# Kernel tuning notes

Hardware: AMD Instinct MI355X
Metric: run time of the kernel (lower is better)

Reference implementation:

```python
import jax, jax.numpy as jnp
import numpy as np

B, N, D = 2, 2048, 1024
H = 16
HD = D // H  # 64
NEG = -1e30


def setup_inputs() -> dict:
    key = jax.random.key(0)
    ks = jax.random.split(key, 6)
    s = 0.02
    return {
        "x": jax.random.normal(ks[0], (B, N, D), dtype=jnp.float32),
        "Wq": jax.random.normal(ks[1], (D, D), dtype=jnp.float32) * s,
        "Wk": jax.random.normal(ks[2], (D, D), dtype=jnp.float32) * s,
        "Wv": jax.random.normal(ks[3], (D, D), dtype=jnp.float32) * s,
        "Wo": jax.random.normal(ks[4], (D, D), dtype=jnp.float32) * s,
        "Wf": jax.random.normal(ks[5], (D, H), dtype=jnp.float32) * s,
    }


def reference(x, Wq, Wk, Wv, Wo, Wf):
    b, n, d = x.shape
    h, hd = H, HD
    scale = hd ** -0.5
    # projections (Linear without bias; weights stored as [in, out])
    q = (x @ Wq).reshape(b, n, h, hd).transpose(0, 2, 1, 3)  # b h n hd
    k = (x @ Wk).reshape(b, n, h, hd).transpose(0, 2, 1, 3)
    v = (x @ Wv).reshape(b, n, h, hd).transpose(0, 2, 1, 3)
    # per-head log forget gate, cumulative sum over positions
    log_f = jax.nn.log_sigmoid(x @ Wf).transpose(0, 2, 1)  # b h n
    c = jnp.cumsum(log_f, axis=-1)  # b h n
    # scores with additive decay bias: bias[i,j] = c[i] - c[j] (j <= i)
    scores = jnp.einsum('bhid,bhjd->bhij', q, k) * scale
    scores = scores + c[..., :, None] - c[..., None, :]
    causal = jnp.tril(jnp.ones((n, n), dtype=bool))
    scores = jnp.where(causal, scores, NEG)
    attn = jax.nn.softmax(scores, axis=-1)
    out = jnp.einsum('bhij,bhjd->bhid', attn, v)  # b h n hd
    out = out.transpose(0, 2, 1, 3).reshape(b, n, d)
    return out @ Wo
```

## Files before the change

### kernel.cpp

```cpp
#include <hip/hip_runtime.h>
#include <hip/hip_bf16.h>
#include <stdint.h>

#define NN 2048
#define DD 1024
#define HH 16
#define HDD 64
#define QBLK 64
#define KVBLK 64

typedef unsigned short u16;
typedef __attribute__((ext_vector_type(8))) __bf16 bf16x8_t;
typedef __attribute__((ext_vector_type(4))) float f32x4_t;

static __device__ __forceinline__ u16 f2bf(float f) {
  union { float f; uint32_t u; } v; v.f = f;
  uint32_t r = v.u + 0x7FFFu + ((v.u >> 16) & 1u);
  return (u16)(r >> 16);
}

static __device__ __forceinline__ uint32_t packbf2(float a, float b) {
  __hip_bfloat162 h2 = __float22bfloat162_rn(make_float2(a, b));
  union { __hip_bfloat162 hh; uint32_t u; } cvt; cvt.hh = h2;
  return cvt.u;
}

static __device__ __forceinline__ void async_copy16(const void* g, void* l) {
  __builtin_amdgcn_global_load_lds((const __attribute__((address_space(1))) void*)g,
                                   (__attribute__((address_space(3))) void*)l, 16, 0, 0);
}

__global__ void transpose_w_kernel(const float* __restrict__ W0, const float* __restrict__ W1,
                                   const float* __restrict__ W2, const float* __restrict__ W3,
                                   u16* __restrict__ Wt) {
  __shared__ float tile[64][65];
  const float* W = blockIdx.y == 0 ? W0 : blockIdx.y == 1 ? W1 : blockIdx.y == 2 ? W2 : W3;
  u16* out = Wt + (size_t)blockIdx.y * DD * DD;
  int bx = blockIdx.x & 15;
  int by = blockIdx.x >> 4;
  int t = threadIdx.x;
  int c = t & 63, r4 = t >> 6;
#pragma unroll
  for (int i = 0; i < 16; i++) {
    int row = i * 4 + r4;
    tile[row][c] = W[(by * 64 + row) * DD + bx * 64 + c];
  }
  __syncthreads();
#pragma unroll
  for (int i = 0; i < 16; i++) {
    int row = i * 4 + r4;
    out[(bx * 64 + row) * DD + by * 64 + c] = f2bf(tile[c][row]);
  }
}

__global__ void logf_kernel(const float* __restrict__ x, const float* __restrict__ Wf,
                            float* __restrict__ lf, u16* __restrict__ xb) {
  __shared__ float xs[DD];
  __shared__ float part[16][17];
  int row = blockIdx.x;
  int t = threadIdx.x;
  float4 v = *(const float4*)&x[(size_t)row * DD + t * 4];
  *(float4*)&xs[t * 4] = v;
  ushort4 o;
  o.x = f2bf(v.x); o.y = f2bf(v.y); o.z = f2bf(v.z); o.w = f2bf(v.w);
  *(ushort4*)&xb[(size_t)row * DD + t * 4] = o;
  __syncthreads();
  int h = t & 15, chunk = t >> 4;
  float s = 0.f;
#pragma unroll 8
  for (int e = 0; e < 64; e++)
    s += xs[chunk * 64 + e] * Wf[(chunk * 64 + e) * HH + h];
  part[chunk][h] = s;
  __syncthreads();
  if (t < 16) {
    float z = 0.f;
#pragma unroll
    for (int i = 0; i < 16; i++) z += part[i][t];
    float ls = fminf(z, 0.f) - log1pf(__expf(-fabsf(z)));
    int b = row >> 11, n = row & (NN - 1);
    lf[(b * HH + t) * NN + n] = ls;
  }
}

__global__ void cumsum_kernel(const float* __restrict__ lf, float* __restrict__ c) {
  int bh = blockIdx.x;
  int lane = threadIdx.x;
  const float* in = lf + bh * NN;
  float* out = c + bh * NN;
  float carry = 0.f;
  for (int t0 = 0; t0 < NN; t0 += 256) {
    float4 v = *(const float4*)&in[t0 + lane * 4];
    float s1 = v.x + v.y, s2 = s1 + v.z, s3 = s2 + v.w;
    float incl = s3;
#pragma unroll
    for (int off = 1; off < 64; off <<= 1) {
      float u = __shfl_up(incl, off, 64);
      if (lane >= off) incl += u;
    }
    float excl = incl - s3 + carry;
    float4 o;
    o.x = excl + v.x; o.y = excl + s1; o.z = excl + s2; o.w = excl + s3;
    *(float4*)&out[t0 + lane * 4] = o;
    carry = __shfl(incl, 63, 64) + carry;
  }
}

__global__ __launch_bounds__(512, 4) void gemm_kernel(const u16* __restrict__ A,
                                                      const u16* __restrict__ Wt,
                                                      u16* __restrict__ oQ, u16* __restrict__ oK,
                                                      u16* __restrict__ oV, float* __restrict__ oF,
                                                      int mode) {
  __shared__ u16 Als[128 * 64];
  __shared__ u16 Bls[128 * 64];
  int m0 = blockIdx.y * 128, n0 = blockIdx.x * 128;
  int tid = threadIdx.x;
  int lane = tid & 63, w = tid >> 6;
  int wm = w >> 2, wn = w & 3;
  int lr = lane & 15, lg = lane >> 4;

  const u16* gA[2]; const u16* gB[2]; u16* lA[2]; u16* lB[2];
#pragma unroll
  for (int j = 0; j < 2; j++) {
    int s = tid + j * 512;
    int row = s >> 3, ch = s & 7;
    int scol = (ch ^ (row & 7)) * 8;
    gA[j] = &A [(size_t)(m0 + row) * DD + scol];
    gB[j] = &Wt[(size_t)(n0 + row) * DD + scol];
    lA[j] = &Als[s * 8];
    lB[j] = &Bls[s * 8];
  }

  f32x4_t acc[4][2];
#pragma unroll
  for (int i = 0; i < 4; i++)
#pragma unroll
    for (int j = 0; j < 2; j++) acc[i][j] = (f32x4_t){0.f, 0.f, 0.f, 0.f};

  for (int kt = 0; kt < DD; kt += 64) {
    __syncthreads();
#pragma unroll
    for (int j = 0; j < 2; j++) {
      async_copy16(gA[j] + kt, lA[j]);
      async_copy16(gB[j] + kt, lB[j]);
    }
    __syncthreads();
#pragma unroll
    for (int kk = 0; kk < 2; kk++) {
      bf16x8_t af[4], bfv[2];
#pragma unroll
      for (int mi = 0; mi < 4; mi++) {
        int row = wm * 64 + mi * 16 + lr;
        int boff = (row * 128 + kk * 64 + lg * 16) ^ ((row & 7) << 4);
        af[mi] = *(const bf16x8_t*)((const char*)Als + boff);
      }
#pragma unroll
      for (int ni = 0; ni < 2; ni++) {
        int row = wn * 32 + ni * 16 + lr;
        int boff = (row * 128 + kk * 64 + lg * 16) ^ ((row & 7) << 4);
        bfv[ni] = *(const bf16x8_t*)((const char*)Bls + boff);
      }
#pragma unroll
      for (int mi = 0; mi < 4; mi++)
#pragma unroll
        for (int ni = 0; ni < 2; ni++)
          acc[mi][ni] = __builtin_amdgcn_mfma_f32_16x16x32_bf16(af[mi], bfv[ni], acc[mi][ni], 0, 0, 0);
    }
  }

  if (mode == 1) {
#pragma unroll
    for (int mi = 0; mi < 4; mi++)
#pragma unroll
      for (int ni = 0; ni < 2; ni++) {
        int gcol = n0 + wn * 32 + ni * 16 + lr;
#pragma unroll
        for (int r = 0; r < 4; r++) {
          int grow = m0 + wm * 64 + mi * 16 + lg * 4 + r;
          oF[(size_t)grow * DD + gcol] = acc[mi][ni][r];
        }
      }
  } else {
    int which = n0 >> 10;
    u16* outp = which == 0 ? oQ : which == 1 ? oK : oV;
    int nl0 = n0 & 1023;
#pragma unroll
    for (int mi = 0; mi < 4; mi++)
#pragma unroll
      for (int ni = 0; ni < 2; ni++) {
        int gcol = nl0 + wn * 32 + ni * 16 + lr;
        int h = gcol >> 6, hd = gcol & 63;
#pragma unroll
        for (int r = 0; r < 4; r++) {
          int grow = m0 + wm * 64 + mi * 16 + lg * 4 + r;
          int b = grow >> 11, n = grow & (NN - 1);
          outp[((size_t)(b * HH + h) * NN + n) * HDD + hd] = f2bf(acc[mi][ni][r]);
        }
      }
  }
}

__global__ void transpose_v_kernel(const u16* __restrict__ Vtmp, u16* __restrict__ Vt) {
  __shared__ u16 tile[64][80];
  int bh = blockIdx.y;
  int n0 = blockIdx.x * 64;
  int t = threadIdx.x;
  const u16* src = Vtmp + (size_t)bh * NN * HDD;
  u16* dst = Vt + (size_t)bh * HDD * NN;
#pragma unroll
  for (int it = 0; it < 2; it++) {
    int cc = t + it * 256;
    int row = cc >> 3, p = cc & 7;
    *(uint4*)&tile[row][p * 8] = *(const uint4*)&src[(size_t)(n0 + row) * HDD + p * 8];
  }
  __syncthreads();
#pragma unroll
  for (int it = 0; it < 2; it++) {
    int cc = t + it * 256;
    int row = cc >> 3, p = cc & 7;
    union { u16 v[8]; uint4 q; } tmp;
#pragma unroll
    for (int e = 0; e < 8; e++) tmp.v[e] = tile[p * 8 + e][row];
    *(uint4*)&dst[(size_t)row * NN + n0 + p * 8] = tmp.q;
  }
}

__global__ __launch_bounds__(256) void attn_kernel(const u16* __restrict__ Q,
                                                   const u16* __restrict__ K,
                                                   const u16* __restrict__ Vt,
                                                   const float* __restrict__ cw,
                                                   u16* __restrict__ O) {
  __shared__ u16 Kls[2][KVBLK * 64];
  __shared__ u16 Vls[2][64 * KVBLK];
  int flat = blockIdx.y * gridDim.x + blockIdx.x;
  int swz = (flat & 7) * 64 + (flat >> 3);
  int pidx = swz & 15, bh = swz >> 4;
  int tid = threadIdx.x;
  int lane = tid & 63, w = tid >> 6;
  int lr = lane & 15, lg = lane >> 4;
  const u16* Qh = Q + (size_t)bh * NN * HDD;
  const u16* Kh = K + (size_t)bh * NN * HDD;
  const u16* Vh = Vt + (size_t)bh * HDD * NN;
  const float* ch = cw + bh * NN;
  int b = bh >> 4, h = bh & 15;

  int s0 = tid, s1 = tid + 256;
  int r0 = s0 >> 3, p0 = s0 & 7;
  int r1 = s1 >> 3, p1 = s1 & 7;
  const u16* gk0 = &Kh[(size_t)r0 * HDD + ((p0 ^ (r0 & 7)) * 8)];
  const u16* gk1 = &Kh[(size_t)r1 * HDD + ((p1 ^ (r1 & 7)) * 8)];
  const u16* gv0 = &Vh[(size_t)r0 * NN + ((p0 ^ (r0 & 7)) * 8)];
  const u16* gv1 = &Vh[(size_t)r1 * NN + ((p1 ^ (r1 & 7)) * 8)];

  for (int which = 0; which < 2; which++) {
    int tile = which == 0 ? (31 - pidx) : pidx;
    int qb = tile * QBLK + w * 16;
    int iq = qb + lr;

    bf16x8_t qf[2];
#pragma unroll
    for (int s = 0; s < 2; s++)
      qf[s] = *(const bf16x8_t*)&Qh[(size_t)iq * HDD + s * 32 + lg * 8];
    float cq = ch[iq];

    float lsum = 0.f;
    f32x4_t oacc[4];
#pragma unroll
    for (int fn = 0; fn < 4; fn++) oacc[fn] = (f32x4_t){0.f, 0.f, 0.f, 0.f};

    async_copy16(gk0, &Kls[0][s0 * 8]);
    async_copy16(gk1, &Kls[0][s1 * 8]);
    async_copy16(gv0, &Vls[0][s0 * 8]);
    async_copy16(gv1, &Vls[0][s1 * 8]);
    __syncthreads();

    int cur = 0;
    for (int kvt = 0; kvt <= tile; kvt++) {
      if (kvt < tile) {
        int nb = cur ^ 1;
        size_t kvn = (size_t)(kvt + 1) * KVBLK;
        async_copy16(gk0 + kvn * HDD, &Kls[nb][s0 * 8]);
        async_copy16(gk1 + kvn * HDD, &Kls[nb][s1 * 8]);
        async_copy16(gv0 + kvn, &Vls[nb][s0 * 8]);
        async_copy16(gv1 + kvn, &Vls[nb][s1 * 8]);
      }
      int kv0 = kvt * KVBLK;
      const u16* Kb = Kls[cur];
      const u16* Vb = Vls[cur];
      float4 ckv[4];
#pragma unroll
      for (int f = 0; f < 4; f++)
        ckv[f] = *(const float4*)&ch[kv0 + f * 16 + lg * 4];

      f32x4_t sacc[4];
#pragma unroll
      for (int f = 0; f < 4; f++) sacc[f] = (f32x4_t){0.f, 0.f, 0.f, 0.f};
      __builtin_amdgcn_s_setprio(1);
#pragma unroll
      for (int f = 0; f < 4; f++) {
        int row = f * 16 + lr;
#pragma unroll
        for (int s = 0; s < 2; s++) {
          int boff = (row * 128 + s * 64 + lg * 16) ^ ((row & 7) << 4);
          bf16x8_t kf = *(const bf16x8_t*)((const char*)Kb + boff);
          sacc[f] = __builtin_amdgcn_mfma_f32_16x16x32_bf16(kf, qf[s], sacc[f], 0, 0, 0);
        }
      }
      __builtin_amdgcn_s_setprio(0);

      bool diag = (kvt == tile);
      float pv[4][4];
#pragma unroll
      for (int f = 0; f < 4; f++) {
        const float* ckp = &ckv[f].x;
#pragma unroll
        for (int r = 0; r < 4; r++) {
          float val = fmaf(sacc[f][r], 0.125f, cq - ckp[r]);
          float e = __expf(val);
          if (diag && (kv0 + f * 16 + lg * 4 + r) > iq) e = 0.f;
          pv[f][r] = e; lsum += e;
        }
      }

      uint32_t wq[4][2];
#pragma unroll
      for (int f = 0; f < 4; f++) {
        wq[f][0] = packbf2(pv[f][0], pv[f][1]);
        wq[f][1] = packbf2(pv[f][2], pv[f][3]);
      }
      bf16x8_t pa[2];
#pragma unroll
      for (int s = 0; s < 2; s++) {
        uint32_t x0 = wq[2 * s][0], x1 = wq[2 * s][1];
        uint32_t y0 = wq[2 * s + 1][0], y1 = wq[2 * s + 1][1];
        asm volatile("v_permlane32_swap_b32 %0, %1" : "+v"(x0), "+v"(y0));
        asm volatile("v_permlane32_swap_b32 %0, %1" : "+v"(x1), "+v"(y1));
        asm volatile("v_permlane16_swap_b32 %0, %1" : "+v"(x0), "+v"(y0));
        asm volatile("v_permlane16_swap_b32 %0, %1" : "+v"(x1), "+v"(y1));
        union { uint32_t u[4]; bf16x8_t v; } pk;
        pk.u[0] = x0; pk.u[1] = x1; pk.u[2] = y0; pk.u[3] = y1;
        pa[s] = pk.v;
      }

      __builtin_amdgcn_s_setprio(1);
#pragma unroll
      for (int fn = 0; fn < 4; fn++) {
        int row = fn * 16 + lr;
#pragma unroll
        for (int s = 0; s < 2; s++) {
          int boff = (row * 128 + s * 64 + lg * 16) ^ ((row & 7) << 4);
          bf16x8_t vf = *(const bf16x8_t*)((const char*)Vb + boff);
          oacc[fn] = __builtin_amdgcn_mfma_f32_16x16x32_bf16(vf, pa[s], oacc[fn], 0, 0, 0);
        }
      }
      __builtin_amdgcn_s_setprio(0);
      __syncthreads();
      cur ^= 1;
    }

    lsum += __shfl_xor(lsum, 16, 64);
    lsum += __shfl_xor(lsum, 32, 64);
    float rinv = 1.0f / lsum;

    u16* orow = O + ((size_t)(b * NN + iq)) * DD + h * HDD;
#pragma unroll
    for (int fn = 0; fn < 4; fn++) {
      ushort4 o4;
      o4.x = f2bf(oacc[fn][0] * rinv);
      o4.y = f2bf(oacc[fn][1] * rinv);
      o4.z = f2bf(oacc[fn][2] * rinv);
      o4.w = f2bf(oacc[fn][3] * rinv);
      *(ushort4*)&orow[fn * 16 + lg * 4] = o4;
    }
  }
}

extern "C" void kernel_launch(void* const* d_in, const int* in_sizes, int n_in,
                              void* d_out, int out_size, void* d_ws, size_t ws_size,
                              hipStream_t stream) {
  const float* x  = (const float*)d_in[0];
  const float* Wq = (const float*)d_in[1];
  const float* Wk = (const float*)d_in[2];
  const float* Wv = (const float*)d_in[3];
  const float* Wo = (const float*)d_in[4];
  const float* Wf = (const float*)d_in[5];
  float* out = (float*)d_out;
  char* ws = (char*)d_ws;
  const size_t MB = 1024 * 1024;
  u16* x_bf  = (u16*)(ws + 0);
  u16* WqkvT = (u16*)(ws + 8 * MB);
  u16* WoT   = (u16*)(ws + 14 * MB);
  u16* Qw    = (u16*)(ws + 16 * MB);
  u16* Kw    = (u16*)(ws + 24 * MB);
  u16* Vw    = (u16*)(ws + 32 * MB);
  u16* Ow    = (u16*)(ws + 40 * MB);
  float* lf  = (float*)(ws + 48 * MB);
  float* cwp = (float*)(ws + 48 * MB + 262144);
  u16* Vtmp  = (u16*)(ws + 49 * MB);

  transpose_w_kernel<<<dim3(256, 4), 256, 0, stream>>>(Wq, Wk, Wv, Wo, WqkvT);
  logf_kernel<<<4096, 256, 0, stream>>>(x, Wf, lf, x_bf);
  cumsum_kernel<<<32, 64, 0, stream>>>(lf, cwp);
  gemm_kernel<<<dim3(24, 32), 512, 0, stream>>>(x_bf, WqkvT, Qw, Kw, Vtmp, nullptr, 0);
  transpose_v_kernel<<<dim3(32, 32), 256, 0, stream>>>(Vtmp, Vw);
  attn_kernel<<<dim3(16, 32), 256, 0, stream>>>(Qw, Kw, Vw, cwp, Ow);
  gemm_kernel<<<dim3(8, 32), 512, 0, stream>>>(Ow, WqkvT + (size_t)3 * DD * DD, nullptr, nullptr, nullptr, out, 1);
}
```

Before: 129.8 us.

## Share K/V tiles across paired query blocks, fuse V transpose into GEMM, use exp2

The attention kernel now processes its two paired query tiles (high and low) in one pass over K/V. The shared prefix tiles are loaded into LDS once and feed MFMAs for both query sets, which removes the redundant K/V reload of the earlier sequential loop. The QKV GEMM epilogue writes V directly in transposed layout, so the separate transpose kernel and its launch go away. The cumulative gate and the score scale are pre-multiplied by log2(e) so exp2f can replace __expf. The costs are higher register pressure from the two accumulator sets and strided 8-byte stores for V.

```diff
diff --git a/kernel.cpp b/kernel.cpp
--- a/kernel.cpp
+++ b/kernel.cpp
@@ -6,12 +6,13 @@
 #define DD 1024
 #define HH 16
 #define HDD 64
-#define QBLK 64
 #define KVBLK 64
 
 typedef unsigned short u16;
 typedef __attribute__((ext_vector_type(8))) __bf16 bf16x8_t;
 typedef __attribute__((ext_vector_type(4))) float f32x4_t;
+
+#define LOG2E 1.44269504f
 
 static __device__ __forceinline__ u16 f2bf(float f) {
   union { float f; uint32_t u; } v; v.f = f;
@@ -23,6 +24,23 @@
   __hip_bfloat162 h2 = __float22bfloat162_rn(make_float2(a, b));
   union { __hip_bfloat162 hh; uint32_t u; } cvt; cvt.hh = h2;
   return cvt.u;
+}
+
+static __device__ __forceinline__ void make_pa(const float pv[4][4], bf16x8_t pa[2]) {
+#pragma unroll
+  for (int s = 0; s < 2; s++) {
+    uint32_t x0 = packbf2(pv[2 * s][0], pv[2 * s][1]);
+    uint32_t x1 = packbf2(pv[2 * s][2], pv[2 * s][3]);
+    uint32_t y0 = packbf2(pv[2 * s + 1][0], pv[2 * s + 1][1]);
+    uint32_t y1 = packbf2(pv[2 * s + 1][2], pv[2 * s + 1][3]);
+    asm volatile("v_permlane32_swap_b32 %0, %1" : "+v"(x0), "+v"(y0));
+    asm volatile("v_permlane32_swap_b32 %0, %1" : "+v"(x1), "+v"(y1));
+    asm volatile("v_permlane16_swap_b32 %0, %1" : "+v"(x0), "+v"(y0));
+    asm volatile("v_permlane16_swap_b32 %0, %1" : "+v"(x1), "+v"(y1));
+    union { uint32_t u[4]; bf16x8_t v; } pk;
+    pk.u[0] = x0; pk.u[1] = x1; pk.u[2] = y0; pk.u[3] = y1;
+    pa[s] = pk.v;
+  }
 }
 
 static __device__ __forceinline__ void async_copy16(const void* g, void* l) {
@@ -99,7 +117,8 @@
     }
     float excl = incl - s3 + carry;
     float4 o;
-    o.x = excl + v.x; o.y = excl + s1; o.z = excl + s2; o.w = excl + s3;
+    o.x = (excl + v.x) * LOG2E; o.y = (excl + s1) * LOG2E;
+    o.z = (excl + s2) * LOG2E; o.w = (excl + s3) * LOG2E;
     *(float4*)&out[t0 + lane * 4] = o;
     carry = __shfl(incl, 63, 64) + carry;
   }
@@ -181,46 +200,39 @@
       }
   } else {
     int which = n0 >> 10;
-    u16* outp = which == 0 ? oQ : which == 1 ? oK : oV;
     int nl0 = n0 & 1023;
-#pragma unroll
-    for (int mi = 0; mi < 4; mi++)
-#pragma unroll
-      for (int ni = 0; ni < 2; ni++) {
-        int gcol = nl0 + wn * 32 + ni * 16 + lr;
-        int h = gcol >> 6, hd = gcol & 63;
-#pragma unroll
-        for (int r = 0; r < 4; r++) {
-          int grow = m0 + wm * 64 + mi * 16 + lg * 4 + r;
-          int b = grow >> 11, n = grow & (NN - 1);
-          outp[((size_t)(b * HH + h) * NN + n) * HDD + hd] = f2bf(acc[mi][ni][r]);
+    if (which == 2) {
+#pragma unroll
+      for (int mi = 0; mi < 4; mi++)
+#pragma unroll
+        for (int ni = 0; ni < 2; ni++) {
+          int gcol = nl0 + wn * 32 + ni * 16 + lr;
+          int h = gcol >> 6, hd = gcol & 63;
+          int grow0 = m0 + wm * 64 + mi * 16 + lg * 4;
+          int b = grow0 >> 11, n = grow0 & (NN - 1);
+          ushort4 o4;
+          o4.x = f2bf(acc[mi][ni][0]);
+          o4.y = f2bf(acc[mi][ni][1]);
+          o4.z = f2bf(acc[mi][ni][2]);
+          o4.w = f2bf(acc[mi][ni][3]);
+          *(ushort4*)&oV[((size_t)(b * HH + h) * HDD + hd) * NN + n] = o4;
         }
-      }
-  }
-}
-
-__global__ void transpose_v_kernel(const u16* __restrict__ Vtmp, u16* __restrict__ Vt) {
-  __shared__ u16 tile[64][80];
-  int bh = blockIdx.y;
-  int n0 = blockIdx.x * 64;
-  int t = threadIdx.x;
-  const u16* src = Vtmp + (size_t)bh * NN * HDD;
-  u16* dst = Vt + (size_t)bh * HDD * NN;
-#pragma unroll
-  for (int it = 0; it < 2; it++) {
-    int cc = t + it * 256;
-    int row = cc >> 3, p = cc & 7;
-    *(uint4*)&tile[row][p * 8] = *(const uint4*)&src[(size_t)(n0 + row) * HDD + p * 8];
-  }
-  __syncthreads();
-#pragma unroll
-  for (int it = 0; it < 2; it++) {
-    int cc = t + it * 256;
-    int row = cc >> 3, p = cc & 7;
-    union { u16 v[8]; uint4 q; } tmp;
-#pragma unroll
-    for (int e = 0; e < 8; e++) tmp.v[e] = tile[p * 8 + e][row];
-    *(uint4*)&dst[(size_t)row * NN + n0 + p * 8] = tmp.q;
+    } else {
+      u16* outp = which == 0 ? oQ : oK;
+#pragma unroll
+      for (int mi = 0; mi < 4; mi++)
+#pragma unroll
+        for (int ni = 0; ni < 2; ni++) {
+          int gcol = nl0 + wn * 32 + ni * 16 + lr;
+          int h = gcol >> 6, hd = gcol & 63;
+#pragma unroll
+          for (int r = 0; r < 4; r++) {
+            int grow = m0 + wm * 64 + mi * 16 + lg * 4 + r;
+            int b = grow >> 11, n = grow & (NN - 1);
+            outp[((size_t)(b * HH + h) * NN + n) * HDD + hd] = f2bf(acc[mi][ni][r]);
+          }
+        }
+    }
   }
 }
 
@@ -243,6 +255,11 @@
   const float* ch = cw + bh * NN;
   int b = bh >> 4, h = bh & 15;
 
+  int th = 31 - pidx, tl = pidx;
+  int qbH = th * 64 + w * 16, qbL = tl * 64 + w * 16;
+  int iqH = qbH + lr, iqL = qbL + lr;
+  int ntiles = th + 1;
+
   int s0 = tid, s1 = tid + 256;
   int r0 = s0 >> 3, p0 = s0 & 7;
   int r1 = s1 >> 3, p1 = s1 & 7;
@@ -251,126 +268,193 @@
   const u16* gv0 = &Vh[(size_t)r0 * NN + ((p0 ^ (r0 & 7)) * 8)];
   const u16* gv1 = &Vh[(size_t)r1 * NN + ((p1 ^ (r1 & 7)) * 8)];
 
-  for (int which = 0; which < 2; which++) {
-    int tile = which == 0 ? (31 - pidx) : pidx;
-    int qb = tile * QBLK + w * 16;
-    int iq = qb + lr;
-
-    bf16x8_t qf[2];
-#pragma unroll
-    for (int s = 0; s < 2; s++)
-      qf[s] = *(const bf16x8_t*)&Qh[(size_t)iq * HDD + s * 32 + lg * 8];
-    float cq = ch[iq];
-
-    float lsum = 0.f;
-    f32x4_t oacc[4];
-#pragma unroll
-    for (int fn = 0; fn < 4; fn++) oacc[fn] = (f32x4_t){0.f, 0.f, 0.f, 0.f};
-
-    async_copy16(gk0, &Kls[0][s0 * 8]);
-    async_copy16(gk1, &Kls[0][s1 * 8]);
-    async_copy16(gv0, &Vls[0][s0 * 8]);
-    async_copy16(gv1, &Vls[0][s1 * 8]);
+  bf16x8_t qfH[2], qfL[2];
+#pragma unroll
+  for (int s = 0; s < 2; s++) {
+    qfH[s] = *(const bf16x8_t*)&Qh[(size_t)iqH * HDD + s * 32 + lg * 8];
+    qfL[s] = *(const bf16x8_t*)&Qh[(size_t)iqL * HDD + s * 32 + lg * 8];
+  }
+  float cqH = ch[iqH], cqL = ch[iqL];
+
+  float lsumH = 0.f, lsumL = 0.f;
+  f32x4_t oaccH[4], oaccL[4];
+#pragma unroll
+  for (int fn = 0; fn < 4; fn++) {
+    oaccH[fn] = (f32x4_t){0.f, 0.f, 0.f, 0.f};
+    oaccL[fn] = (f32x4_t){0.f, 0.f, 0.f, 0.f};
+  }
+
+  const float SCL = 0.125f * LOG2E;
+
+  async_copy16(gk0, &Kls[0][s0 * 8]);
+  async_copy16(gk1, &Kls[0][s1 * 8]);
+  async_copy16(gv0, &Vls[0][s0 * 8]);
+  async_copy16(gv1, &Vls[0][s1 * 8]);
+  __syncthreads();
+
+  int cur = 0;
+  int kvt = 0;
+
+  for (; kvt <= tl; kvt++) {
+    if (kvt + 1 < ntiles) {
+      size_t kvn = (size_t)(kvt + 1) * KVBLK;
+      async_copy16(gk0 + kvn * HDD, &Kls[cur ^ 1][s0 * 8]);
+      async_copy16(gk1 + kvn * HDD, &Kls[cur ^ 1][s1 * 8]);
+      async_copy16(gv0 + kvn, &Vls[cur ^ 1][s0 * 8]);
+      async_copy16(gv1 + kvn, &Vls[cur ^ 1][s1 * 8]);
+    }
+    int kv0 = kvt * KVBLK;
+    const u16* Kb = Kls[cur];
+    const u16* Vb = Vls[cur];
+    float4 ckv[4];
+#pragma unroll
+    for (int f = 0; f < 4; f++)
+      ckv[f] = *(const float4*)&ch[kv0 + f * 16 + lg * 4];
+
+    f32x4_t saH[4], saL[4];
+#pragma unroll
+    for (int f = 0; f < 4; f++) {
+      saH[f] = (f32x4_t){0.f, 0.f, 0.f, 0.f};
+      saL[f] = (f32x4_t){0.f, 0.f, 0.f, 0.f};
+    }
+    __builtin_amdgcn_s_setprio(1);
+#pragma unroll
+    for (int f = 0; f < 4; f++) {
+      int row = f * 16 + lr;
+#pragma unroll
+      for (int s = 0; s < 2; s++) {
+        int boff = (row * 128 + s * 64 + lg * 16) ^ ((row & 7) << 4);
+        bf16x8_t kf = *(const bf16x8_t*)((const char*)Kb + boff);
+        saH[f] = __builtin_amdgcn_mfma_f32_16x16x32_bf16(kf, qfH[s], saH[f], 0, 0, 0);
+        saL[f] = __builtin_amdgcn_mfma_f32_16x16x32_bf16(kf, qfL[s], saL[f], 0, 0, 0);
+      }
+    }
+    __builtin_amdgcn_s_setprio(0);
+
+    bool diagL = (kvt == tl);
+    float pvH[4][4], pvL[4][4];
+#pragma unroll
+    for (int f = 0; f < 4; f++) {
+      const float* ckp = &ckv[f].x;
+#pragma unroll
+      for (int r = 0; r < 4; r++) {
+        int jj = kv0 + f * 16 + lg * 4 + r;
+        float eH = exp2f(fmaf(saH[f][r], SCL, cqH - ckp[r]));
+        float eL = exp2f(fmaf(saL[f][r], SCL, cqL - ckp[r]));
+        if (diagL && jj > iqL) eL = 0.f;
+        pvH[f][r] = eH; lsumH += eH;
+        pvL[f][r] = eL; lsumL += eL;
+      }
+    }
+
+    bf16x8_t paH[2], paL[2];
+    make_pa(pvH, paH);
+    make_pa(pvL, paL);
+
+    __builtin_amdgcn_s_setprio(1);
+#pragma unroll
+    for (int fn = 0; fn < 4; fn++) {
+      int row = fn * 16 + lr;
+#pragma unroll
+      for (int s = 0; s < 2; s++) {
+        int boff = (row * 128 + s * 64 + lg * 16) ^ ((row & 7) << 4);
+        bf16x8_t vf = *(const bf16x8_t*)((const char*)Vb + boff);
+        oaccH[fn] = __builtin_amdgcn_mfma_f32_16x16x32_bf16(vf, paH[s], oaccH[fn], 0, 0, 0);
+        oaccL[fn] = __builtin_amdgcn_mfma_f32_16x16x32_bf16(vf, paL[s], oaccL[fn], 0, 0, 0);
+      }
+    }
+    __builtin_amdgcn_s_setprio(0);
     __syncthreads();
-
-    int cur = 0;
-    for (int kvt = 0; kvt <= tile; kvt++) {
-      if (kvt < tile) {
-        int nb = cur ^ 1;
-        size_t kvn = (size_t)(kvt + 1) * KVBLK;
-        async_copy16(gk0 + kvn * HDD, &Kls[nb][s0 * 8]);
-        async_copy16(gk1 + kvn * HDD, &Kls[nb][s1 * 8]);
-        async_copy16(gv0 + kvn, &Vls[nb][s0 * 8]);
-        async_copy16(gv1 + kvn, &Vls[nb][s1 * 8]);
-      }
-      int kv0 = kvt * KVBLK;
-      const u16* Kb = Kls[cur];
-      const u16* Vb = Vls[cur];
-      float4 ckv[4];
-#pragma unroll
-      for (int f = 0; f < 4; f++)
-        ckv[f] = *(const float4*)&ch[kv0 + f * 16 + lg * 4];
-
-      f32x4_t sacc[4];
-#pragma unroll
-      for (int f = 0; f < 4; f++) sacc[f] = (f32x4_t){0.f, 0.f, 0.f, 0.f};
-      __builtin_amdgcn_s_setprio(1);
-#pragma unroll
-      for (int f = 0; f < 4; f++) {
-        int row = f * 16 + lr;
-#pragma unroll
-        for (int s = 0; s < 2; s++) {
-          int boff = (row * 128 + s * 64 + lg * 16) ^ ((row & 7) << 4);
-          bf16x8_t kf = *(const bf16x8_t*)((const char*)Kb + boff);
-          sacc[f] = __builtin_amdgcn_mfma_f32_16x16x32_bf16(kf, qf[s], sacc[f], 0, 0, 0);
-        }
-      }
-      __builtin_amdgcn_s_setprio(0);
-
-      bool diag = (kvt == tile);
-      float pv[4][4];
-#pragma unroll
-      for (int f = 0; f < 4; f++) {
-        const float* ckp = &ckv[f].x;
-#pragma unroll
-        for (int r = 0; r < 4; r++) {
-          float val = fmaf(sacc[f][r], 0.125f, cq - ckp[r]);
-          float e = __expf(val);
-          if (diag && (kv0 + f * 16 + lg * 4 + r) > iq) e = 0.f;
-          pv[f][r] = e; lsum += e;
-        }
-      }
-
-      uint32_t wq[4][2];
-#pragma unroll
-      for (int f = 0; f < 4; f++) {
-        wq[f][0] = packbf2(pv[f][0], pv[f][1]);
-        wq[f][1] = packbf2(pv[f][2], pv[f][3]);
-      }
-      bf16x8_t pa[2];
+    cur ^= 1;
+  }
+
+  for (; kvt < ntiles; kvt++) {
+    if (kvt + 1 < ntiles) {
+      size_t kvn = (size_t)(kvt + 1) * KVBLK;
+      async_copy16(gk0 + kvn * HDD, &Kls[cur ^ 1][s0 * 8]);
+      async_copy16(gk1 + kvn * HDD, &Kls[cur ^ 1][s1 * 8]);
+      async_copy16(gv0 + kvn, &Vls[cur ^ 1][s0 * 8]);
+      async_copy16(gv1 + kvn, &Vls[cur ^ 1][s1 * 8]);
+    }
+    int kv0 = kvt * KVBLK;
+    const u16* Kb = Kls[cur];
+    const u16* Vb = Vls[cur];
+    float4 ckv[4];
+#pragma unroll
+    for (int f = 0; f < 4; f++)
+      ckv[f] = *(const float4*)&ch[kv0 + f * 16 + lg * 4];
+
+    f32x4_t saH[4];
+#pragma unroll
+    for (int f = 0; f < 4; f++) saH[f] = (f32x4_t){0.f, 0.f, 0.f, 0.f};
+    __builtin_amdgcn_s_setprio(1);
+#pragma unroll
+    for (int f = 0; f < 4; f++) {
+      int row = f * 16 + lr;
 #pragma unroll
       for (int s = 0; s < 2; s++) {
-        uint32_t x0 = wq[2 * s][0], x1 = wq[2 * s][1];
-        uint32_t y0 = wq[2 * s + 1][0], y1 = wq[2 * s + 1][1];
-        asm volatile("v_permlane32_swap_b32 %0, %1" : "+v"(x0), "+v"(y0));
-        asm volatile("v_permlane32_swap_b32 %0, %1" : "+v"(x1), "+v"(y1));
-        asm volatile("v_permlane16_swap_b32 %0, %1" : "+v"(x0), "+v"(y0));
-        asm volatile("v_permlane16_swap_b32 %0, %1" : "+v"(x1), "+v"(y1));
-        union { uint32_t u[4]; bf16x8_t v; } pk;
-        pk.u[0] = x0; pk.u[1] = x1; pk.u[2] = y0; pk.u[3] = y1;
-        pa[s] = pk.v;
-      }
-
-      __builtin_amdgcn_s_setprio(1);
-#pragma unroll
-      for (int fn = 0; fn < 4; fn++) {
-        int row = fn * 16 + lr;
-#pragma unroll
-        for (int s = 0; s < 2; s++) {
-          int boff = (row * 128 + s * 64 + lg * 16) ^ ((row & 7) << 4);
-          bf16x8_t vf = *(const bf16x8_t*)((const char*)Vb + boff);
-          oacc[fn] = __builtin_amdgcn_mfma_f32_16x16x32_bf16(vf, pa[s], oacc[fn], 0, 0, 0);
-        }
-      }
-      __builtin_amdgcn_s_setprio(0);
-      __syncthreads();
-      cur ^= 1;
-    }
-
-    lsum += __shfl_xor(lsum, 16, 64);
-    lsum += __shfl_xor(lsum, 32, 64);
-    float rinv = 1.0f / lsum;
-
-    u16* orow = O + ((size_t)(b * NN + iq)) * DD + h * HDD;
+        int boff = (row * 128 + s * 64 + lg * 16) ^ ((row & 7) << 4);
+        bf16x8_t kf = *(const bf16x8_t*)((const char*)Kb + boff);
+        saH[f] = __builtin_amdgcn_mfma_f32_16x16x32_bf16(kf, qfH[s], saH[f], 0, 0, 0);
+      }
+    }
+    __builtin_amdgcn_s_setprio(0);
+
+    bool diag = (kvt == th);
+    float pvH[4][4];
+#pragma unroll
+    for (int f = 0; f < 4; f++) {
+      const float* ckp = &ckv[f].x;
+#pragma unroll
+      for (int r = 0; r < 4; r++) {
+        int jj = kv0 + f * 16 + lg * 4 + r;
+        float eH = exp2f(fmaf(saH[f][r], SCL, cqH - ckp[r]));
+        if (diag && jj > iqH) eH = 0.f;
+        pvH[f][r] = eH; lsumH += eH;
+      }
+    }
+
+    bf16x8_t paH[2];
+    make_pa(pvH, paH);
+
+    __builtin_amdgcn_s_setprio(1);
 #pragma unroll
     for (int fn = 0; fn < 4; fn++) {
-      ushort4 o4;
-      o4.x = f2bf(oacc[fn][0] * rinv);
-      o4.y = f2bf(oacc[fn][1] * rinv);
-      o4.z = f2bf(oacc[fn][2] * rinv);
-      o4.w = f2bf(oacc[fn][3] * rinv);
-      *(ushort4*)&orow[fn * 16 + lg * 4] = o4;
-    }
+      int row = fn * 16 + lr;
+#pragma unroll
+      for (int s = 0; s < 2; s++) {
+        int boff = (row * 128 + s * 64 + lg * 16) ^ ((row & 7) << 4);
+        bf16x8_t vf = *(const bf16x8_t*)((const char*)Vb + boff);
+        oaccH[fn] = __builtin_amdgcn_mfma_f32_16x16x32_bf16(vf, paH[s], oaccH[fn], 0, 0, 0);
+      }
+    }
+    __builtin_amdgcn_s_setprio(0);
+    __syncthreads();
+    cur ^= 1;
+  }
+
+  lsumH += __shfl_xor(lsumH, 16, 64);
+  lsumH += __shfl_xor(lsumH, 32, 64);
+  lsumL += __shfl_xor(lsumL, 16, 64);
+  lsumL += __shfl_xor(lsumL, 32, 64);
+  float rinvH = 1.0f / lsumH, rinvL = 1.0f / lsumL;
+
+  u16* orowH = O + ((size_t)(b * NN + iqH)) * DD + h * HDD;
+  u16* orowL = O + ((size_t)(b * NN + iqL)) * DD + h * HDD;
+#pragma unroll
+  for (int fn = 0; fn < 4; fn++) {
+    ushort4 o4;
+    o4.x = f2bf(oaccH[fn][0] * rinvH);
+    o4.y = f2bf(oaccH[fn][1] * rinvH);
+    o4.z = f2bf(oaccH[fn][2] * rinvH);
+    o4.w = f2bf(oaccH[fn][3] * rinvH);
+    *(ushort4*)&orowH[fn * 16 + lg * 4] = o4;
+    ushort4 o5;
+    o5.x = f2bf(oaccL[fn][0] * rinvL);
+    o5.y = f2bf(oaccL[fn][1] * rinvL);
+    o5.z = f2bf(oaccL[fn][2] * rinvL);
+    o5.w = f2bf(oaccL[fn][3] * rinvL);
+    *(ushort4*)&orowL[fn * 16 + lg * 4] = o5;
   }
 }
 
@@ -395,13 +479,11 @@
   u16* Ow    = (u16*)(ws + 40 * MB);
   float* lf  = (float*)(ws + 48 * MB);
   float* cwp = (float*)(ws + 48 * MB + 262144);
-  u16* Vtmp  = (u16*)(ws + 49 * MB);
 
   transpose_w_kernel<<<dim3(256, 4), 256, 0, stream>>>(Wq, Wk, Wv, Wo, WqkvT);
   logf_kernel<<<4096, 256, 0, stream>>>(x, Wf, lf, x_bf);
   cumsum_kernel<<<32, 64, 0, stream>>>(lf, cwp);
-  gemm_kernel<<<dim3(24, 32), 512, 0, stream>>>(x_bf, WqkvT, Qw, Kw, Vtmp, nullptr, 0);
-  transpose_v_kernel<<<dim3(32, 32), 256, 0, stream>>>(Vtmp, Vw);
+  gemm_kernel<<<dim3(24, 32), 512, 0, stream>>>(x_bf, WqkvT, Qw, Kw, Vw, nullptr, 0);
   attn_kernel<<<dim3(16, 32), 256, 0, stream>>>(Qw, Kw, Vw, cwp, Ow);
   gemm_kernel<<<dim3(8, 32), 512, 0, stream>>>(Ow, WqkvT + (size_t)3 * DD * DD, nullptr, nullptr, nullptr, out, 1);
 }
```

After: 137.6 us. 6.0% more time.
